# Performance work log

Hardware: AMD Instinct MI355X
Metric: run time of the kernel (lower is better)

The kernel has to match this reference:

```python
import jax, jax.numpy as jnp
import numpy as np

B, D, C = 4096, 768, 80
PRIV = np.arange(0, 20)        # privileged label indices
NONPRIV = np.arange(20, 80)    # non-privileged label indices
EPS = 1e-8
BETA = 1.0
EPSILON = 0.1
DIMS = [768, 256, 64, 16, 4, 1]


def setup_inputs() -> dict:
    key = jax.random.key(0)
    ks = jax.random.split(key, 12)
    inp = {
        "hidden": jax.random.normal(ks[0], (B, D), dtype=jnp.float32),
        "labels": jax.random.randint(ks[1], (B, C), 0, 2, dtype=jnp.int32),
    }
    ki = 2
    for wpref, bpref in (("W", "b"), ("rW", "rb")):
        for i in range(5):
            din, dout = DIMS[i], DIMS[i + 1]
            inp[f"{wpref}{i+1}"] = (jax.random.normal(ks[ki], (C, din, dout), dtype=jnp.float32)
                                     * (1.0 / np.sqrt(din)))
            inp[f"{bpref}{i+1}"] = jnp.zeros((C, dout), dtype=jnp.float32)
            ki += 1
    return inp


def _scores(hidden, Ws, bs):
    # c independent MLP heads applied to the same hidden state, batched over c.
    x = jnp.einsum('bd,cdh->bch', hidden, Ws[0]) + bs[0]  # (b, c, 256)
    for W, b in zip(Ws[1:], bs[1:]):
        x = jnp.einsum('bch,cho->bco', jax.nn.relu(x), W) + b
    return jax.nn.sigmoid(x[..., 0])  # (b, c)


def _bce(p, y):
    p = jnp.clip(p, EPS, 1.0 - EPS)
    return -(y * jnp.log(p) + (1.0 - y) * jnp.log1p(-p))


def _losses(scores, ref_scores, labels):
    ref_scores = jax.lax.stop_gradient(ref_scores)  # ref head is frozen
    # --- privileged pairwise margin loss (vectorized masked form) ---
    log_term = jnp.log(scores / (ref_scores + EPS) + EPS)  # (b, c)
    ps = scores[:, PRIV]                                   # (b, P)
    pos = labels[:, PRIV] == 1                             # (b, P)
    neg = labels == 0                                      # (b, c)
    # confusing negative k for positive privileged l: y_k==0 and s_k >= s_l
    conf = pos[:, :, None] & neg[:, None, :] & (scores[:, None, :] >= ps[:, :, None])
    h_w = log_term[:, PRIV][:, :, None] - log_term[:, None, :]   # (b, P, c)
    pair_loss = -jax.nn.log_sigmoid(BETA * h_w)
    n_pairs = conf.sum()
    total = jnp.where(conf, pair_loss, 0.0).sum()
    loss_priv = jnp.where(n_pairs > 0, total / jnp.maximum(n_pairs, 1), 0.0)
    # --- non-privileged hinged BCE ---
    y = labels[:, NONPRIV].astype(jnp.float32)
    loss_cur = _bce(scores[:, NONPRIV], y)
    loss_ref = jax.lax.stop_gradient(_bce(ref_scores[:, NONPRIV], y))
    loss_nonpriv = jnp.mean(jax.nn.relu(loss_cur - loss_ref - EPSILON))
    return jnp.stack([loss_priv, loss_nonpriv])


def reference(hidden, labels, W1, b1, W2, b2, W3, b3, W4, b4, W5, b5,
              rW1, rb1, rW2, rb2, rW3, rb3, rW4, rb4, rW5, rb5):
    scores = _scores(hidden, (W1, W2, W3, W4, W5), (b1, b2, b3, b4, b5))
    ref_scores = _scores(hidden, (rW1, rW2, rW3, rW4, rW5), (rb1, rb2, rb3, rb4, rb5))
    return _losses(scores, ref_scores, labels)
```

## Files before the change

kernel.cpp:

```cpp
#include <hip/hip_runtime.h>
#include <math.h>

typedef __attribute__((ext_vector_type(8))) short short8;
typedef __attribute__((ext_vector_type(4))) float f32x4;

#define Bn   4096
#define Dn   768
#define Cn   80
#define H1   256
#define H2   64
#define H3   16
#define H4   4

__device__ inline ushort f2bf(float f) {
    union { float f; unsigned u; } v; v.f = f;
    unsigned r = v.u + 0x7fffu + ((v.u >> 16) & 1u);
    return (ushort)(r >> 16);
}
__device__ inline unsigned pack2(float a, float b) {
    return (unsigned)f2bf(a) | ((unsigned)f2bf(b) << 16);
}
__device__ inline void load_lds16(const void* g, void* l) {
    __builtin_amdgcn_global_load_lds(
        (const __attribute__((address_space(1))) void*)g,
        (__attribute__((address_space(3))) void*)l, 16, 0, 0);
}

#define FENCE() asm volatile("" ::: "memory")
#define BAR() do { FENCE(); __builtin_amdgcn_sched_barrier(0); \
                   __builtin_amdgcn_s_barrier(); \
                   __builtin_amdgcn_sched_barrier(0); FENCE(); } while (0)
#define VMCNT3() do { asm volatile("s_waitcnt vmcnt(3)" ::: "memory"); \
                      __builtin_amdgcn_sched_barrier(0); } while (0)
#define VMCNT0() do { asm volatile("s_waitcnt vmcnt(0)" ::: "memory"); \
                      __builtin_amdgcn_sched_barrier(0); } while (0)

__global__ __launch_bounds__(256)
void convert_hidden(const float* __restrict__ hidden, ushort* __restrict__ hbs)
{
    const int t = threadIdx.x;
    const int kt = blockIdx.x;
    const int bt = blockIdx.y;
    char* out = (char*)hbs + ((size_t)bt * 24 + kt) * 8192;
    #pragma unroll
    for (int ch = 0; ch < 2; ++ch) {
        const int o = (ch * 256 + t) * 16;
        const int r = o >> 6;
        const int s = (o >> 4) & 3;
        const int k0 = (s ^ (r & 3)) * 8;
        const float* src = hidden + (size_t)(bt * 128 + r) * Dn + kt * 32 + k0;
        const float4 f0 = ((const float4*)src)[0];
        const float4 f1 = ((const float4*)src)[1];
        uint4 w;
        w.x = pack2(f0.x, f0.y); w.y = pack2(f0.z, f0.w);
        w.z = pack2(f1.x, f1.y); w.w = pack2(f1.z, f1.w);
        *(uint4*)(out + o) = w;
    }
}

__global__ __launch_bounds__(256)
void convert_w1(const float* __restrict__ W, const float* __restrict__ rW,
                ushort* __restrict__ dst)
{
    __shared__ float l[32 * H1];
    const int t   = threadIdx.x;
    const int kt2 = blockIdx.x;
    const int c   = blockIdx.y;
    const int set = blockIdx.z;
    const float* src = (set ? rW : W) + ((size_t)c * Dn + kt2 * 32) * H1;
    #pragma unroll
    for (int i = 0; i < 8; ++i)
        ((float4*)l)[i * 256 + t] = ((const float4*)src)[i * 256 + t];
    __syncthreads();
    char* out = (char*)dst + (((size_t)set * Cn + c) * 24 + kt2) * 16384;
    #pragma unroll
    for (int rd = 0; rd < 4; ++rd) {
        const int o = (rd * 256 + t) * 16;
        const int n = o >> 6;
        const int s = (o >> 4) & 3;
        const int kk0 = (s ^ (n & 3)) * 8;
        uint4 w;
        w.x = pack2(l[(kk0 + 0) * H1 + n], l[(kk0 + 1) * H1 + n]);
        w.y = pack2(l[(kk0 + 2) * H1 + n], l[(kk0 + 3) * H1 + n]);
        w.z = pack2(l[(kk0 + 4) * H1 + n], l[(kk0 + 5) * H1 + n]);
        w.w = pack2(l[(kk0 + 6) * H1 + n], l[(kk0 + 7) * H1 + n]);
        *(uint4*)(out + o) = w;
    }
}

__global__ __launch_bounds__(256)
void convert_w23(const float* __restrict__ W2, const float* __restrict__ rW2,
                 const float* __restrict__ W3, const float* __restrict__ rW3,
                 ushort* __restrict__ dstW2, ushort* __restrict__ dstW3)
{
    __shared__ float l[64 * H2];
    const int t   = threadIdx.x;
    const int bx  = blockIdx.x;
    const int c   = blockIdx.y;
    const int set = blockIdx.z;

    if (bx < 4) {
        const float* src = (set ? rW2 : W2) + ((size_t)c * H1 + bx * 64) * H2;
        #pragma unroll
        for (int i = 0; i < 4; ++i)
            ((float4*)l)[i * 256 + t] = ((const float4*)src)[i * 256 + t];
        __syncthreads();
        char* out = (char*)dstW2 + (((size_t)set * Cn + c) * 4 + bx) * 8192;
        #pragma unroll
        for (int rd = 0; rd < 2; ++rd) {
            const int idx = rd * 256 + t;
            const int n = idx >> 3;
            const int s = idx & 7;
            const int o = n * 128 + ((s << 4) ^ ((n & 7) << 4));
            const int kk0 = s * 8;
            uint4 w;
            w.x = pack2(l[(kk0 + 0) * H2 + n], l[(kk0 + 1) * H2 + n]);
            w.y = pack2(l[(kk0 + 2) * H2 + n], l[(kk0 + 3) * H2 + n]);
            w.z = pack2(l[(kk0 + 4) * H2 + n], l[(kk0 + 5) * H2 + n]);
            w.w = pack2(l[(kk0 + 6) * H2 + n], l[(kk0 + 7) * H2 + n]);
            *(uint4*)(out + o) = w;
        }
    } else if (t < 128) {
        const float* src = (set ? rW3 : W3) + (size_t)c * (H2 * H3);
        char* out = (char*)dstW3 + ((size_t)set * Cn + c) * 2048;
        const int o = t * 16;
        const int n = o >> 7;
        const int slot = (o >> 4) & 7;
        const int kk0 = (slot ^ (n & 7)) * 8;
        uint4 w;
        w.x = pack2(src[(kk0 + 0) * H3 + n], src[(kk0 + 1) * H3 + n]);
        w.y = pack2(src[(kk0 + 2) * H3 + n], src[(kk0 + 3) * H3 + n]);
        w.z = pack2(src[(kk0 + 4) * H3 + n], src[(kk0 + 5) * H3 + n]);
        w.w = pack2(src[(kk0 + 6) * H3 + n], src[(kk0 + 7) * H3 + n]);
        *(uint4*)(out + o) = w;
    }
}


__device__ __forceinline__ void stageA(char* lds, const char* hb, int slot, int kt, int t) {
    load_lds16(hb + (size_t)kt * 8192 + t * 16, lds + slot * 8192 + t * 16);
}
__device__ __forceinline__ void stageB(char* lds, const char* w1b, int slot, int kt, int t) {
    const char* g = w1b + (size_t)kt * 16384 + t * 16;
    char* l = lds + 24576 + slot * 16384 + t * 16;
    load_lds16(g,        l);
    load_lds16(g + 8192, l + 8192);
}

__global__ __launch_bounds__(512, 4)
void scores_mfma_128(const ushort* __restrict__ hbs, const ushort* __restrict__ W1ts,
                     const ushort* __restrict__ W2ts, const ushort* __restrict__ W3ts,
                     const float* __restrict__ b1, const float* __restrict__ rb1,
                     const float* __restrict__ b2, const float* __restrict__ rb2,
                     const float* __restrict__ b3, const float* __restrict__ rb3,
                     const float* __restrict__ W4, const float* __restrict__ rW4,
                     const float* __restrict__ b4, const float* __restrict__ rb4,
                     const float* __restrict__ W5, const float* __restrict__ rW5,
                     const float* __restrict__ b5, const float* __restrict__ rb5,
                     float* __restrict__ scores)
{
    __shared__ uint4 smv[73728 / 16];
    char* lds = (char*)smv;

    const int t = threadIdx.x;
    const int wid = t >> 6, lane = t & 63;
    const int lrow = lane & 15;
    const int lkg  = lane >> 4;
    const int lk   = lkg * 8;
    const int wr = wid >> 2, wc = wid & 3;

    const int cpx = 5120 >> 3;
    const int wg  = (blockIdx.x & 7) * cpx + (blockIdx.x >> 3);
    const int set = wg / 2560;
    const int rem = wg % 2560;
    const int c   = rem / 32;
    const int bt  = rem % 32;

    const float* pb1 = set ? rb1 : b1;
    const float* pb2 = set ? rb2 : b2;
    const float* pb3 = set ? rb3 : b3;
    const float* pW4 = set ? rW4 : W4;  const float* pb4 = set ? rb4 : b4;
    const float* pW5 = set ? rW5 : W5;  const float* pb5 = set ? rb5 : b5;

    const char* hb  = (const char*)hbs + (size_t)bt * 196608;
    const char* w1b = (const char*)W1ts + (size_t)(set * Cn + c) * 393216;

    f32x4 acc[4][4];
    #pragma unroll
    for (int i = 0; i < 4; ++i)
        #pragma unroll
        for (int j = 0; j < 4; ++j)
            acc[i][j] = (f32x4){0.f, 0.f, 0.f, 0.f};

    stageA(lds, hb, 0, 0, t);  stageB(lds, w1b, 0, 0, t);
    stageA(lds, hb, 1, 1, t);  stageB(lds, w1b, 1, 1, t);
    VMCNT3();
    BAR();

    #pragma unroll 3
    for (int j = 0; j < 24; ++j) {
        const int rs = j % 3;
        short8 breg[4], areg[4];
        {
            const char* bb = lds + 24576 + rs * 16384;
            const char* ab = lds + rs * 8192;
            #pragma unroll
            for (int nt = 0; nt < 4; ++nt) {
                const int col = wc * 64 + nt * 16 + lrow;
                breg[nt] = *(const short8*)(bb + col * 64 + ((2 * lk) ^ ((col & 3) << 4)));
            }
            #pragma unroll
            for (int mt = 0; mt < 4; ++mt) {
                const int row = wr * 64 + mt * 16 + lrow;
                areg[mt] = *(const short8*)(ab + row * 64 + ((2 * lk) ^ ((row & 3) << 4)));
            }
        }
        {
            const int ws = (j + 2) % 3;
            int ka = j + 2; if (ka >= 24) ka -= 24;
            stageA(lds, hb, ws, ka, t);
            stageB(lds, w1b, ws, ka, t);
        }
        VMCNT3();
        BAR();
        __builtin_amdgcn_s_setprio(1);
        #pragma unroll
        for (int mt = 0; mt < 4; ++mt)
            #pragma unroll
            for (int nt = 0; nt < 4; ++nt)
                acc[mt][nt] = __builtin_amdgcn_mfma_f32_16x16x32_bf16(
                    breg[nt], areg[mt], acc[mt][nt], 0, 0, 0);
        __builtin_amdgcn_s_setprio(0);
        BAR();
    }
    VMCNT0();
    BAR();

    {
        float4 bias1[4];
        #pragma unroll
        for (int nt = 0; nt < 4; ++nt)
            bias1[nt] = *(const float4*)&pb1[(size_t)c * H1 + wc * 64 + nt * 16 + lkg * 4];
        #pragma unroll
        for (int mt = 0; mt < 4; ++mt) {
            const int row = wr * 64 + mt * 16 + lrow;
            const int swz = (row & 7) << 4;
            #pragma unroll
            for (int nt = 0; nt < 4; ++nt) {
                const float* bb = (const float*)&bias1[nt];
                uint2 w;
                w.x = pack2(fmaxf(acc[mt][nt][0] + bb[0], 0.f),
                            fmaxf(acc[mt][nt][1] + bb[1], 0.f));
                w.y = pack2(fmaxf(acc[mt][nt][2] + bb[2], 0.f),
                            fmaxf(acc[mt][nt][3] + bb[3], 0.f));
                const int off = row * 512 + ((wc * 128 + nt * 32 + lkg * 8) ^ swz);
                *(uint2*)(lds + off) = w;
            }
        }
    }
    BAR();

    f32x4 acc2[4];
    #pragma unroll
    for (int j = 0; j < 4; ++j) acc2[j] = (f32x4){0.f, 0.f, 0.f, 0.f};
    {
        const char* w2b = (const char*)W2ts + (size_t)(set * Cn + c) * 32768;
        const int row = wid * 16 + lrow;
        const int swzr = (row & 7) << 4;
        #pragma unroll
        for (int ksz = 0; ksz < 8; ++ksz) {
            short8 b2r[4];
            const int kk2 = (ksz & 1) * 32 + lk;
            #pragma unroll
            for (int nt = 0; nt < 4; ++nt) {
                const int col = nt * 16 + lrow;
                b2r[nt] = *(const short8*)(w2b + (ksz >> 1) * 8192
                             + ((col * 128 + 2 * kk2) ^ ((col & 7) << 4)));
            }
            const int k = ksz * 32 + lk;
            const short8 a2 = *(const short8*)(lds + ((row * 512 + 2 * k) ^ swzr));
            #pragma unroll
            for (int nt = 0; nt < 4; ++nt)
                acc2[nt] = __builtin_amdgcn_mfma_f32_16x16x32_bf16(
                    b2r[nt], a2, acc2[nt], 0, 0, 0);
        }
    }
    BAR();

    {
        const int row = wid * 16 + lrow;
        const int swz = (row & 7) << 4;
        #pragma unroll
        for (int nt = 0; nt < 4; ++nt) {
            const float4 bv = *(const float4*)&pb2[(size_t)c * H2 + nt * 16 + lkg * 4];
            const float* bb = (const float*)&bv;
            uint2 w;
            w.x = pack2(fmaxf(acc2[nt][0] + bb[0], 0.f),
                        fmaxf(acc2[nt][1] + bb[1], 0.f));
            w.y = pack2(fmaxf(acc2[nt][2] + bb[2], 0.f),
                        fmaxf(acc2[nt][3] + bb[3], 0.f));
            const int off = row * 128 + ((nt * 32 + lkg * 8) ^ swz);
            *(uint2*)(lds + off) = w;
        }
    }
    BAR();

    {
        const char* w3t = (const char*)W3ts + (size_t)(set * Cn + c) * 2048;
        short8 w3f[2];
        #pragma unroll
        for (int ks = 0; ks < 2; ++ks)
            w3f[ks] = *(const short8*)(w3t + lrow * 128
                         + ((2 * (ks * 32 + lk)) ^ ((lrow & 7) << 4)));
        f32x4 acc3 = (f32x4){0.f, 0.f, 0.f, 0.f};
        const int row = wid * 16 + lrow;
        #pragma unroll
        for (int ks = 0; ks < 2; ++ks) {
            const short8 xf = *(const short8*)(lds + row * 128
                                 + ((2 * (ks * 32 + lk)) ^ ((row & 7) << 4)));
            acc3 = __builtin_amdgcn_mfma_f32_16x16x32_bf16(w3f[ks], xf, acc3, 0, 0, 0);
        }

        const float4 b3v = *(const float4*)&pb3[(size_t)c * H3 + lkg * 4];
        const float* w4c = pW4 + (size_t)c * (H3 * H4);
        float4 w4r[4];
        #pragma unroll
        for (int r = 0; r < 4; ++r)
            w4r[r] = *(const float4*)&w4c[(lkg * 4 + r) * H4];
        const float4 b4v = *(const float4*)&pb4[(size_t)c * H4];
        const float4 w5v = *(const float4*)&pW5[(size_t)c * H4];
        const float bb5 = pb5[c];

        float p4[4] = {0.f, 0.f, 0.f, 0.f};
        #pragma unroll
        for (int r = 0; r < 4; ++r) {
            const float x3 = fmaxf(acc3[r] + ((const float*)&b3v)[r], 0.f);
            const float* wr4 = (const float*)&w4r[r];
            #pragma unroll
            for (int o = 0; o < 4; ++o)
                p4[o] = fmaf(x3, wr4[o], p4[o]);
        }
        #pragma unroll
        for (int o = 0; o < 4; ++o) {
            p4[o] += __shfl_xor(p4[o], 16, 64);
            p4[o] += __shfl_xor(p4[o], 32, 64);
        }
        float x5 = bb5;
        #pragma unroll
        for (int o = 0; o < 4; ++o)
            x5 = fmaf(fmaxf(p4[o] + ((const float*)&b4v)[o], 0.f),
                      ((const float*)&w5v)[o], x5);
        const float sc = 1.f / (1.f + expf(-x5));
        if (lkg == 0)
            scores[((size_t)set * Bn + bt * 128 + wid * 16 + lrow) * Cn + c] = sc;
    }
}

__device__ inline float bce_f(float p, float y) {
    p = fminf(fmaxf(p, 1e-8f), 1.0f - 1e-8f);
    return -(y * logf(p) + (1.f - y) * log1pf(-p));
}

__global__ __launch_bounds__(128)
void loss_kernel(const float* __restrict__ scores, const int* __restrict__ labels,
                 float* __restrict__ pair_sum, float* __restrict__ np_sum,
                 int* __restrict__ pair_cnt)
{
    __shared__ float ss[Cn], lt[Cn];
    __shared__ int lab[Cn];
    __shared__ float redf[128], redn[128];
    __shared__ int redi[128];

    const int b = blockIdx.x, t = threadIdx.x;
    float np_local = 0.f, ps_local = 0.f;
    int pc_local = 0;

    if (t < Cn) {
        const float s  = scores[(size_t)b * Cn + t];
        const float sr = scores[(size_t)Bn * Cn + (size_t)b * Cn + t];
        const int l = labels[(size_t)b * Cn + t];
        ss[t] = s; lab[t] = l;
        lt[t] = logf(s / (sr + 1e-8f) + 1e-8f);
        if (t >= 20) {
            const float y = (float)l;
            np_local = fmaxf(bce_f(s, y) - bce_f(sr, y) - 0.1f, 0.f);
        }
    }
    __syncthreads();
    if (t < Cn && lab[t] == 0) {
        const float sj = ss[t], ltj = lt[t];
        #pragma unroll
        for (int i = 0; i < 20; ++i) {
            if (lab[i] == 1 && sj >= ss[i]) {
                const float z = -(lt[i] - ltj);
                ps_local += fmaxf(z, 0.f) + log1pf(expf(-fabsf(z)));
                pc_local++;
            }
        }
    }
    redf[t] = ps_local; redn[t] = np_local; redi[t] = pc_local;
    __syncthreads();
    for (int s = 64; s > 0; s >>= 1) {
        if (t < s) { redf[t] += redf[t + s]; redn[t] += redn[t + s]; redi[t] += redi[t + s]; }
        __syncthreads();
    }
    if (t == 0) { pair_sum[b] = redf[0]; np_sum[b] = redn[0]; pair_cnt[b] = redi[0]; }
}

__global__ __launch_bounds__(1024)
void final_kernel(const float* __restrict__ pair_sum, const int* __restrict__ pair_cnt,
                  const float* __restrict__ np_sum, float* __restrict__ out)
{
    __shared__ float r1[1024], r2[1024];
    __shared__ int ri[1024];
    const int t = threadIdx.x;
    float s1 = 0.f, s2 = 0.f; int c1 = 0;
    for (int i = t; i < Bn; i += 1024) { s1 += pair_sum[i]; c1 += pair_cnt[i]; s2 += np_sum[i]; }
    r1[t] = s1; r2[t] = s2; ri[t] = c1;
    __syncthreads();
    for (int s = 512; s > 0; s >>= 1) {
        if (t < s) { r1[t] += r1[t + s]; r2[t] += r2[t + s]; ri[t] += ri[t + s]; }
        __syncthreads();
    }
    if (t == 0) {
        const int n = ri[0];
        out[0] = (n > 0) ? (r1[0] / (float)(n > 1 ? n : 1)) : 0.f;
        out[1] = r2[0] / (float)(Bn * 60);
    }
}

static inline size_t alup(size_t x) { return (x + 4095) & ~(size_t)4095; }

extern "C" void kernel_launch(void* const* d_in, const int* in_sizes, int n_in,
                              void* d_out, int out_size, void* d_ws, size_t ws_size,
                              hipStream_t stream)
{
    const float* hidden = (const float*)d_in[0];
    const int*   labels = (const int*)d_in[1];
    const float* W1 = (const float*)d_in[2];   const float* b1 = (const float*)d_in[3];
    const float* W2 = (const float*)d_in[4];   const float* b2 = (const float*)d_in[5];
    const float* W3 = (const float*)d_in[6];   const float* b3 = (const float*)d_in[7];
    const float* W4 = (const float*)d_in[8];   const float* b4 = (const float*)d_in[9];
    const float* W5 = (const float*)d_in[10];  const float* b5 = (const float*)d_in[11];
    const float* rW1 = (const float*)d_in[12]; const float* rb1 = (const float*)d_in[13];
    const float* rW2 = (const float*)d_in[14]; const float* rb2 = (const float*)d_in[15];
    const float* rW3 = (const float*)d_in[16]; const float* rb3 = (const float*)d_in[17];
    const float* rW4 = (const float*)d_in[18]; const float* rb4 = (const float*)d_in[19];
    const float* rW5 = (const float*)d_in[20]; const float* rb5 = (const float*)d_in[21];

    char* ws = (char*)d_ws;
    const size_t off_scores = 0;
    const size_t sz_scores  = (size_t)2 * Bn * Cn * 4;
    const size_t off_pair   = alup(off_scores + sz_scores);
    const size_t sz_pair    = (size_t)3 * Bn * 4;
    const size_t off_hbs    = alup(off_pair + sz_pair);
    const size_t sz_hbs     = (size_t)Bn * Dn * 2;
    const size_t off_w1t    = alup(off_hbs + sz_hbs);
    const size_t sz_w1t     = (size_t)2 * Cn * 24 * 16384;
    const size_t off_w2t    = alup(off_w1t + sz_w1t);
    const size_t sz_w2t     = (size_t)2 * Cn * 4 * 8192;
    const size_t off_w3t    = alup(off_w2t + sz_w2t);

    float* scoresb  = (float*)(ws + off_scores);
    float* pair_sum = (float*)(ws + off_pair);
    float* np_sum   = pair_sum + Bn;
    int*   pair_cnt = (int*)(np_sum + Bn);
    float* out      = (float*)d_out;

    ushort* hbs  = (ushort*)(ws + off_hbs);
    ushort* W1ts = (ushort*)(ws + off_w1t);
    ushort* W2ts = (ushort*)(ws + off_w2t);
    ushort* W3ts = (ushort*)(ws + off_w3t);

    convert_hidden<<<dim3(24, Bn / 128), 256, 0, stream>>>(hidden, hbs);
    convert_w1<<<dim3(24, Cn, 2), 256, 0, stream>>>(W1, rW1, W1ts);
    convert_w23<<<dim3(5, Cn, 2), 256, 0, stream>>>(W2, rW2, W3, rW3, W2ts, W3ts);

    scores_mfma_128<<<5120, 512, 0, stream>>>(hbs, W1ts, W2ts, W3ts,
        b1, rb1, b2, rb2, b3, rb3, W4, rW4, b4, rb4, W5, rW5, b5, rb5,
        scoresb);
    loss_kernel<<<Bn, 128, 0, stream>>>(scoresb, labels, pair_sum, np_sum, pair_cnt);
    final_kernel<<<1, 1024, 0, stream>>>(pair_sum, pair_cnt, np_sum, out);
}
```

Before: 378.4 us.

## Halve workgroup to 4 waves with 64x128 per-wave tiles and new LDS swizzle

The main scores kernel now runs 256 threads (4 waves) per block instead of 512, so each wave computes a 64x128 tile of the first layer (32 accumulators) rather than 64x64, and handles 32 rows in the later layers. The wider per-wave tile raises MFMA work per LDS fragment read and cuts the number of waves contending for the barrier. Each thread now issues twice as many global-to-LDS loads, and the wait count is adjusted to match. The LDS XOR swizzle changes from row&3 to (row>>1)&3, in both the conversion kernels and the readers, to reduce bank conflicts. The cost is more registers per wave and lower occupancy (launch bounds 256,2), which gives less latency hiding.

```diff
diff --git a/kernel.cpp b/kernel.cpp
--- a/kernel.cpp
+++ b/kernel.cpp
@@ -30,7 +30,7 @@
 #define BAR() do { FENCE(); __builtin_amdgcn_sched_barrier(0); \
                    __builtin_amdgcn_s_barrier(); \
                    __builtin_amdgcn_sched_barrier(0); FENCE(); } while (0)
-#define VMCNT3() do { asm volatile("s_waitcnt vmcnt(3)" ::: "memory"); \
+#define VMCNT6() do { asm volatile("s_waitcnt vmcnt(6)" ::: "memory"); \
                       __builtin_amdgcn_sched_barrier(0); } while (0)
 #define VMCNT0() do { asm volatile("s_waitcnt vmcnt(0)" ::: "memory"); \
                       __builtin_amdgcn_sched_barrier(0); } while (0)
@@ -47,7 +47,7 @@
         const int o = (ch * 256 + t) * 16;
         const int r = o >> 6;
         const int s = (o >> 4) & 3;
-        const int k0 = (s ^ (r & 3)) * 8;
+        const int k0 = (s ^ ((r >> 1) & 3)) * 8;
         const float* src = hidden + (size_t)(bt * 128 + r) * Dn + kt * 32 + k0;
         const float4 f0 = ((const float4*)src)[0];
         const float4 f1 = ((const float4*)src)[1];
@@ -78,7 +78,7 @@
         const int o = (rd * 256 + t) * 16;
         const int n = o >> 6;
         const int s = (o >> 4) & 3;
-        const int kk0 = (s ^ (n & 3)) * 8;
+        const int kk0 = (s ^ ((n >> 1) & 3)) * 8;
         uint4 w;
         w.x = pack2(l[(kk0 + 0) * H1 + n], l[(kk0 + 1) * H1 + n]);
         w.y = pack2(l[(kk0 + 2) * H1 + n], l[(kk0 + 3) * H1 + n]);
@@ -138,26 +138,31 @@
 
 
 __device__ __forceinline__ void stageA(char* lds, const char* hb, int slot, int kt, int t) {
-    load_lds16(hb + (size_t)kt * 8192 + t * 16, lds + slot * 8192 + t * 16);
+    const char* g = hb + (size_t)kt * 8192 + t * 16;
+    char* l = lds + slot * 8192 + t * 16;
+    load_lds16(g,        l);
+    load_lds16(g + 4096, l + 4096);
 }
 __device__ __forceinline__ void stageB(char* lds, const char* w1b, int slot, int kt, int t) {
     const char* g = w1b + (size_t)kt * 16384 + t * 16;
     char* l = lds + 24576 + slot * 16384 + t * 16;
-    load_lds16(g,        l);
-    load_lds16(g + 8192, l + 8192);
-}
-
-__global__ __launch_bounds__(512, 4)
-void scores_mfma_128(const ushort* __restrict__ hbs, const ushort* __restrict__ W1ts,
-                     const ushort* __restrict__ W2ts, const ushort* __restrict__ W3ts,
-                     const float* __restrict__ b1, const float* __restrict__ rb1,
-                     const float* __restrict__ b2, const float* __restrict__ rb2,
-                     const float* __restrict__ b3, const float* __restrict__ rb3,
-                     const float* __restrict__ W4, const float* __restrict__ rW4,
-                     const float* __restrict__ b4, const float* __restrict__ rb4,
-                     const float* __restrict__ W5, const float* __restrict__ rW5,
-                     const float* __restrict__ b5, const float* __restrict__ rb5,
-                     float* __restrict__ scores)
+    load_lds16(g,         l);
+    load_lds16(g + 4096,  l + 4096);
+    load_lds16(g + 8192,  l + 8192);
+    load_lds16(g + 12288, l + 12288);
+}
+
+__global__ __launch_bounds__(256, 2)
+void scores_mfma_w128(const ushort* __restrict__ hbs, const ushort* __restrict__ W1ts,
+                      const ushort* __restrict__ W2ts, const ushort* __restrict__ W3ts,
+                      const float* __restrict__ b1, const float* __restrict__ rb1,
+                      const float* __restrict__ b2, const float* __restrict__ rb2,
+                      const float* __restrict__ b3, const float* __restrict__ rb3,
+                      const float* __restrict__ W4, const float* __restrict__ rW4,
+                      const float* __restrict__ b4, const float* __restrict__ rb4,
+                      const float* __restrict__ W5, const float* __restrict__ rW5,
+                      const float* __restrict__ b5, const float* __restrict__ rb5,
+                      float* __restrict__ scores)
 {
     __shared__ uint4 smv[73728 / 16];
     char* lds = (char*)smv;
@@ -167,7 +172,8 @@
     const int lrow = lane & 15;
     const int lkg  = lane >> 4;
     const int lk   = lkg * 8;
-    const int wr = wid >> 2, wc = wid & 3;
+    const int wr  = wid >> 1;
+    const int wcn = wid & 1;
 
     const int cpx = 5120 >> 3;
     const int wg  = (blockIdx.x & 7) * cpx + (blockIdx.x >> 3);
@@ -185,34 +191,36 @@
     const char* hb  = (const char*)hbs + (size_t)bt * 196608;
     const char* w1b = (const char*)W1ts + (size_t)(set * Cn + c) * 393216;
 
-    f32x4 acc[4][4];
+    f32x4 acc[4][8];
     #pragma unroll
     for (int i = 0; i < 4; ++i)
         #pragma unroll
-        for (int j = 0; j < 4; ++j)
+        for (int j = 0; j < 8; ++j)
             acc[i][j] = (f32x4){0.f, 0.f, 0.f, 0.f};
 
     stageA(lds, hb, 0, 0, t);  stageB(lds, w1b, 0, 0, t);
     stageA(lds, hb, 1, 1, t);  stageB(lds, w1b, 1, 1, t);
-    VMCNT3();
+    VMCNT6();
     BAR();
 
     #pragma unroll 3
     for (int j = 0; j < 24; ++j) {
         const int rs = j % 3;
-        short8 breg[4], areg[4];
+        short8 breg[8], areg[4];
         {
             const char* bb = lds + 24576 + rs * 16384;
             const char* ab = lds + rs * 8192;
             #pragma unroll
-            for (int nt = 0; nt < 4; ++nt) {
-                const int col = wc * 64 + nt * 16 + lrow;
-                breg[nt] = *(const short8*)(bb + col * 64 + ((2 * lk) ^ ((col & 3) << 4)));
+            for (int nt = 0; nt < 8; ++nt) {
+                const int col = wcn * 128 + nt * 16 + lrow;
+                breg[nt] = *(const short8*)(bb + col * 64
+                              + ((2 * lk) ^ (((col >> 1) & 3) << 4)));
             }
             #pragma unroll
             for (int mt = 0; mt < 4; ++mt) {
                 const int row = wr * 64 + mt * 16 + lrow;
-                areg[mt] = *(const short8*)(ab + row * 64 + ((2 * lk) ^ ((row & 3) << 4)));
+                areg[mt] = *(const short8*)(ab + row * 64
+                              + ((2 * lk) ^ (((row >> 1) & 3) << 4)));
             }
         }
         {
@@ -221,13 +229,13 @@
             stageA(lds, hb, ws, ka, t);
             stageB(lds, w1b, ws, ka, t);
         }
-        VMCNT3();
+        VMCNT6();
         BAR();
         __builtin_amdgcn_s_setprio(1);
         #pragma unroll
         for (int mt = 0; mt < 4; ++mt)
             #pragma unroll
-            for (int nt = 0; nt < 4; ++nt)
+            for (int nt = 0; nt < 8; ++nt)
                 acc[mt][nt] = __builtin_amdgcn_mfma_f32_16x16x32_bf16(
                     breg[nt], areg[mt], acc[mt][nt], 0, 0, 0);
         __builtin_amdgcn_s_setprio(0);
@@ -237,39 +245,40 @@
     BAR();
 
     {
-        float4 bias1[4];
-        #pragma unroll
-        for (int nt = 0; nt < 4; ++nt)
-            bias1[nt] = *(const float4*)&pb1[(size_t)c * H1 + wc * 64 + nt * 16 + lkg * 4];
+        float4 bias1[8];
+        #pragma unroll
+        for (int nt = 0; nt < 8; ++nt)
+            bias1[nt] = *(const float4*)&pb1[(size_t)c * H1 + wcn * 128 + nt * 16 + lkg * 4];
         #pragma unroll
         for (int mt = 0; mt < 4; ++mt) {
             const int row = wr * 64 + mt * 16 + lrow;
             const int swz = (row & 7) << 4;
             #pragma unroll
-            for (int nt = 0; nt < 4; ++nt) {
+            for (int nt = 0; nt < 8; ++nt) {
                 const float* bb = (const float*)&bias1[nt];
                 uint2 w;
                 w.x = pack2(fmaxf(acc[mt][nt][0] + bb[0], 0.f),
                             fmaxf(acc[mt][nt][1] + bb[1], 0.f));
                 w.y = pack2(fmaxf(acc[mt][nt][2] + bb[2], 0.f),
                             fmaxf(acc[mt][nt][3] + bb[3], 0.f));
-                const int off = row * 512 + ((wc * 128 + nt * 32 + lkg * 8) ^ swz);
+                const int off = row * 512 + ((wcn * 256 + nt * 32 + lkg * 8) ^ swz);
                 *(uint2*)(lds + off) = w;
             }
         }
     }
     BAR();
 
-    f32x4 acc2[4];
+    f32x4 acc2[2][4];
     #pragma unroll
-    for (int j = 0; j < 4; ++j) acc2[j] = (f32x4){0.f, 0.f, 0.f, 0.f};
+    for (int i = 0; i < 2; ++i)
+        #pragma unroll
+        for (int j = 0; j < 4; ++j)
+            acc2[i][j] = (f32x4){0.f, 0.f, 0.f, 0.f};
     {
         const char* w2b = (const char*)W2ts + (size_t)(set * Cn + c) * 32768;
-        const int row = wid * 16 + lrow;
-        const int swzr = (row & 7) << 4;
         #pragma unroll
         for (int ksz = 0; ksz < 8; ++ksz) {
-            short8 b2r[4];
+            short8 b2r[4], a2[2];
             const int kk2 = (ksz & 1) * 32 + lk;
             #pragma unroll
             for (int nt = 0; nt < 4; ++nt) {
@@ -278,29 +287,41 @@
                              + ((col * 128 + 2 * kk2) ^ ((col & 7) << 4)));
             }
             const int k = ksz * 32 + lk;
-            const short8 a2 = *(const short8*)(lds + ((row * 512 + 2 * k) ^ swzr));
-            #pragma unroll
-            for (int nt = 0; nt < 4; ++nt)
-                acc2[nt] = __builtin_amdgcn_mfma_f32_16x16x32_bf16(
-                    b2r[nt], a2, acc2[nt], 0, 0, 0);
+            #pragma unroll
+            for (int m2 = 0; m2 < 2; ++m2) {
+                const int row = wid * 32 + m2 * 16 + lrow;
+                a2[m2] = *(const short8*)(lds + ((row * 512 + 2 * k) ^ ((row & 7) << 4)));
+            }
+            #pragma unroll
+            for (int m2 = 0; m2 < 2; ++m2)
+                #pragma unroll
+                for (int nt = 0; nt < 4; ++nt)
+                    acc2[m2][nt] = __builtin_amdgcn_mfma_f32_16x16x32_bf16(
+                        b2r[nt], a2[m2], acc2[m2][nt], 0, 0, 0);
         }
     }
     BAR();
 
     {
-        const int row = wid * 16 + lrow;
-        const int swz = (row & 7) << 4;
-        #pragma unroll
-        for (int nt = 0; nt < 4; ++nt) {
-            const float4 bv = *(const float4*)&pb2[(size_t)c * H2 + nt * 16 + lkg * 4];
-            const float* bb = (const float*)&bv;
-            uint2 w;
-            w.x = pack2(fmaxf(acc2[nt][0] + bb[0], 0.f),
-                        fmaxf(acc2[nt][1] + bb[1], 0.f));
-            w.y = pack2(fmaxf(acc2[nt][2] + bb[2], 0.f),
-                        fmaxf(acc2[nt][3] + bb[3], 0.f));
-            const int off = row * 128 + ((nt * 32 + lkg * 8) ^ swz);
-            *(uint2*)(lds + off) = w;
+        float4 bias2[4];
+        #pragma unroll
+        for (int nt = 0; nt < 4; ++nt)
+            bias2[nt] = *(const float4*)&pb2[(size_t)c * H2 + nt * 16 + lkg * 4];
+        #pragma unroll
+        for (int m2 = 0; m2 < 2; ++m2) {
+            const int row = wid * 32 + m2 * 16 + lrow;
+            const int swz = (row & 7) << 4;
+            #pragma unroll
+            for (int nt = 0; nt < 4; ++nt) {
+                const float* bb = (const float*)&bias2[nt];
+                uint2 w;
+                w.x = pack2(fmaxf(acc2[m2][nt][0] + bb[0], 0.f),
+                            fmaxf(acc2[m2][nt][1] + bb[1], 0.f));
+                w.y = pack2(fmaxf(acc2[m2][nt][2] + bb[2], 0.f),
+                            fmaxf(acc2[m2][nt][3] + bb[3], 0.f));
+                const int off = row * 128 + ((nt * 32 + lkg * 8) ^ swz);
+                *(uint2*)(lds + off) = w;
+            }
         }
     }
     BAR();
@@ -312,13 +333,19 @@
         for (int ks = 0; ks < 2; ++ks)
             w3f[ks] = *(const short8*)(w3t + lrow * 128
                          + ((2 * (ks * 32 + lk)) ^ ((lrow & 7) << 4)));
-        f32x4 acc3 = (f32x4){0.f, 0.f, 0.f, 0.f};
-        const int row = wid * 16 + lrow;
-        #pragma unroll
-        for (int ks = 0; ks < 2; ++ks) {
-            const short8 xf = *(const short8*)(lds + row * 128
-                                 + ((2 * (ks * 32 + lk)) ^ ((row & 7) << 4)));
-            acc3 = __builtin_amdgcn_mfma_f32_16x16x32_bf16(w3f[ks], xf, acc3, 0, 0, 0);
+        f32x4 acc3[2];
+        #pragma unroll
+        for (int m2 = 0; m2 < 2; ++m2) acc3[m2] = (f32x4){0.f, 0.f, 0.f, 0.f};
+        #pragma unroll
+        for (int m2 = 0; m2 < 2; ++m2) {
+            const int row = wid * 32 + m2 * 16 + lrow;
+            #pragma unroll
+            for (int ks = 0; ks < 2; ++ks) {
+                const short8 xf = *(const short8*)(lds + row * 128
+                                     + ((2 * (ks * 32 + lk)) ^ ((row & 7) << 4)));
+                acc3[m2] = __builtin_amdgcn_mfma_f32_16x16x32_bf16(
+                    w3f[ks], xf, acc3[m2], 0, 0, 0);
+            }
         }
 
         const float4 b3v = *(const float4*)&pb3[(size_t)c * H3 + lkg * 4];
@@ -331,28 +358,31 @@
         const float4 w5v = *(const float4*)&pW5[(size_t)c * H4];
         const float bb5 = pb5[c];
 
-        float p4[4] = {0.f, 0.f, 0.f, 0.f};
-        #pragma unroll
-        for (int r = 0; r < 4; ++r) {
-            const float x3 = fmaxf(acc3[r] + ((const float*)&b3v)[r], 0.f);
-            const float* wr4 = (const float*)&w4r[r];
+        #pragma unroll
+        for (int m2 = 0; m2 < 2; ++m2) {
+            float p4[4] = {0.f, 0.f, 0.f, 0.f};
+            #pragma unroll
+            for (int r = 0; r < 4; ++r) {
+                const float x3 = fmaxf(acc3[m2][r] + ((const float*)&b3v)[r], 0.f);
+                const float* wr4 = (const float*)&w4r[r];
+                #pragma unroll
+                for (int o = 0; o < 4; ++o)
+                    p4[o] = fmaf(x3, wr4[o], p4[o]);
+            }
+            #pragma unroll
+            for (int o = 0; o < 4; ++o) {
+                p4[o] += __shfl_xor(p4[o], 16, 64);
+                p4[o] += __shfl_xor(p4[o], 32, 64);
+            }
+            float x5 = bb5;
             #pragma unroll
             for (int o = 0; o < 4; ++o)
-                p4[o] = fmaf(x3, wr4[o], p4[o]);
-        }
-        #pragma unroll
-        for (int o = 0; o < 4; ++o) {
-            p4[o] += __shfl_xor(p4[o], 16, 64);
-            p4[o] += __shfl_xor(p4[o], 32, 64);
-        }
-        float x5 = bb5;
-        #pragma unroll
-        for (int o = 0; o < 4; ++o)
-            x5 = fmaf(fmaxf(p4[o] + ((const float*)&b4v)[o], 0.f),
-                      ((const float*)&w5v)[o], x5);
-        const float sc = 1.f / (1.f + expf(-x5));
-        if (lkg == 0)
-            scores[((size_t)set * Bn + bt * 128 + wid * 16 + lrow) * Cn + c] = sc;
+                x5 = fmaf(fmaxf(p4[o] + ((const float*)&b4v)[o], 0.f),
+                          ((const float*)&w5v)[o], x5);
+            const float sc = 1.f / (1.f + expf(-x5));
+            if (lkg == 0)
+                scores[((size_t)set * Bn + bt * 128 + wid * 32 + m2 * 16 + lrow) * Cn + c] = sc;
+        }
     }
 }
 
@@ -476,7 +506,7 @@
     convert_w1<<<dim3(24, Cn, 2), 256, 0, stream>>>(W1, rW1, W1ts);
     convert_w23<<<dim3(5, Cn, 2), 256, 0, stream>>>(W2, rW2, W3, rW3, W2ts, W3ts);
 
-    scores_mfma_128<<<5120, 512, 0, stream>>>(hbs, W1ts, W2ts, W3ts,
+    scores_mfma_w128<<<5120, 256, 0, stream>>>(hbs, W1ts, W2ts, W3ts,
         b1, rb1, b2, rb2, b3, rb3, W4, rW4, b4, rb4, W5, rW5, b5, rb5,
         scoresb);
     loss_kernel<<<Bn, 128, 0, stream>>>(scoresb, labels, pair_sum, np_sum, pair_cnt);
```

After: 340.1 us. -10.1%, faster.
